# Optimization experiments

Hardware: AMD Instinct MI355X
Metric: run time of the kernel (lower is better)

Reference implementation:

```python
import jax, jax.numpy as jnp
import numpy as np

N_NODES = 16
N_EDGES = 64
N_LAYERS = 4


def _gcn(x, src, dst, emask, W, b):
    # PyG GCNConv: add self-loops, symmetric deg^-1/2 normalization, sum-aggregate.
    n = x.shape[0]
    h = x @ W  # [n, d_out]
    deg = jax.ops.segment_sum(emask, dst, num_segments=n) + 1.0  # +1 self-loop
    dinv = jax.lax.rsqrt(deg)
    norm = dinv[src] * dinv[dst] * emask  # masked-out edges get 0 weight
    out = jax.ops.segment_sum(norm[:, None] * h[src], dst, num_segments=n)
    return out + (dinv * dinv)[:, None] * h + b  # self-loop term + bias


def _sag_pool(x, src, dst, emask, w_rel, b_rel, w_root, k):
    # SAGPooling with GraphConv scorer: score = lin_rel(sum_j x_j) + lin_root(x)
    n = x.shape[0]
    agg = jax.ops.segment_sum(emask[:, None] * x[src], dst, num_segments=n)
    score = agg @ w_rel + b_rel + x @ w_root  # [n]
    perm = jnp.argsort(-score)[:k]  # top-k nodes
    x_new = x[perm] * jnp.tanh(score[perm])[:, None]
    kept = jnp.zeros(n, bool).at[perm].set(True)
    pos = jnp.zeros(n, jnp.int32).at[perm].set(jnp.arange(k, dtype=jnp.int32))
    emask_new = emask * kept[src] * kept[dst]  # drop edges touching removed nodes
    return x_new, pos[src], pos[dst], emask_new


def _conv_gnn(x, src, dst, W0, Ws, bs, pWrel, pbrel, pWroot, linW, linb):
    emask = jnp.ones(src.shape[0], x.dtype)
    n = x.shape[0]
    for i in range(N_LAYERS):
        W = W0 if i == 0 else Ws[i - 1]
        x = jax.nn.relu(_gcn(x, src, dst, emask, W, bs[i]))
        k = -(-n // 2)  # ceil(0.5 * n) -- SAGPooling ratio=0.5
        x, src, dst, emask = _sag_pool(x, src, dst, emask, pWrel[i], pbrel[i], pWroot[i], k)
        n = k
    x = x @ linW + linb  # [1, 128]
    return jax.nn.log_softmax(x, axis=1)


def _fc(h, fcW, fcb, lnw, lnb):
    eps = 1e-5
    for i in range(3):
        h = h @ fcW[i] + fcb[i]
        mu = h.mean(-1, keepdims=True)
        var = ((h - mu) ** 2).mean(-1, keepdims=True)
        h = (h - mu) * jax.lax.rsqrt(var + eps) * lnw[i] + lnb[i]
        h = jax.nn.relu(h)
    return h @ fcW[3] + fcb[3]


def setup_inputs() -> dict:
    key = jax.random.key(0)
    ks = iter(jax.random.split(key, 64))

    def rn(shape, s=0.05):
        return jax.random.normal(next(ks), shape, jnp.float32) * s

    def gnn_params(p):
        return {
            p + '_W0': rn((45, 128)), p + '_W': rn((3, 128, 128)),
            p + '_b': jnp.zeros((4, 128), jnp.float32),
            p + '_pWrel': rn((4, 128)), p + '_pbrel': jnp.zeros((4,), jnp.float32),
            p + '_pWroot': rn((4, 128)),
            p + '_linW': rn((128, 128)), p + '_linb': jnp.zeros((128,), jnp.float32),
        }

    inp = {
        'gp_x': rn((N_NODES, 45), 1.0), 'sp_x': rn((N_NODES, 45), 1.0),
        'gp_src': jax.random.randint(next(ks), (N_EDGES,), 0, N_NODES, jnp.int32),
        'gp_dst': jax.random.randint(next(ks), (N_EDGES,), 0, N_NODES, jnp.int32),
        'sp_src': jax.random.randint(next(ks), (N_EDGES,), 0, N_NODES, jnp.int32),
        'sp_dst': jax.random.randint(next(ks), (N_EDGES,), 0, N_NODES, jnp.int32),
        'fcW': rn((4, 256, 256)), 'fcb': jnp.zeros((4, 256), jnp.float32),
        'lnw': jnp.ones((3, 256), jnp.float32), 'lnb': jnp.zeros((3, 256), jnp.float32),
    }
    inp.update(gnn_params('g'))
    inp.update(gnn_params('s'))
    return inp


def reference(gp_x, sp_x, gp_src, gp_dst, sp_src, sp_dst,
              g_W0, g_W, g_b, g_pWrel, g_pbrel, g_pWroot, g_linW, g_linb,
              s_W0, s_W, s_b, s_pWrel, s_pbrel, s_pWroot, s_linW, s_linb,
              fcW, fcb, lnw, lnb):
    out1 = _conv_gnn(gp_x, gp_src, gp_dst, g_W0, g_W, g_b, g_pWrel, g_pbrel, g_pWroot, g_linW, g_linb)
    out2 = _conv_gnn(sp_x, sp_src, sp_dst, s_W0, s_W, s_b, s_pWrel, s_pbrel, s_pWroot, s_linW, s_linb)
    concat = jnp.concatenate((out1.reshape(-1), out2.reshape(-1)))  # [256]
    return _fc(concat, fcW, fcb, lnw, lnb)
```

## Files before the change

### kernel.cpp

```cpp
#include <hip/hip_runtime.h>
#include <math.h>

#define MAGIC 0x5F3759DFu
typedef unsigned int u32;

__device__ __forceinline__ void bar_lds(){
  asm volatile("s_waitcnt lgkmcnt(0)\n\ts_barrier" ::: "memory");
}
__device__ __forceinline__ void bar_vm0(){
  asm volatile("s_waitcnt vmcnt(0) lgkmcnt(0)\n\ts_barrier" ::: "memory");
}
__device__ __forceinline__ void bar_vm8(){
  asm volatile("s_waitcnt vmcnt(8) lgkmcnt(0)\n\ts_barrier" ::: "memory");
}

__device__ inline float wsum(float v){
  #pragma unroll
  for (int o=32;o;o>>=1) v += __shfl_xor(v,o,64);
  return v;
}
__device__ inline float wmax(float v){
  #pragma unroll
  for (int o=32;o;o>>=1) v = fmaxf(v,__shfl_xor(v,o,64));
  return v;
}
__device__ inline float hsum32(float v){
  #pragma unroll
  for (int o=16;o;o>>=1) v += __shfl_xor(v,o,64);
  return v;
}
__device__ __forceinline__ void stageW(const float* g, float* l, int nfloats,
                                       int wid, int lane){
  const int nch = nfloats>>8;
  for (int c=wid; c<nch; c+=8)
    __builtin_amdgcn_global_load_lds(
      (__attribute__((address_space(1))) u32*)(void*)(g+(c<<8)+(lane<<2)),
      (__attribute__((address_space(3))) u32*)(void*)(l+(c<<8)), 16, 0, 0);
}
__device__ __forceinline__ void pf(const float* p, int nfloats, int tid){
  float4 acc={0.f,0.f,0.f,0.f};
  const int nq=nfloats>>2;
  for (int i=tid;i<nq;i+=512){
    const float4 v=((const float4*)p)[i];
    acc.x+=v.x; acc.y+=v.y; acc.z+=v.z; acc.w+=v.w;
  }
  asm volatile("" :: "v"(acc.x),"v"(acc.y),"v"(acc.z),"v"(acc.w));
}

template<int L>
__device__ __forceinline__ void cfused(int lt, const float* slot, const float* ZBp,
    float (*XB)[128], const float* wrelL, const float* wrootL,
    float4 blv, float* d1P, float* d2P){
  const int SPL=1<<L, CH=128>>L;
  const int o=lt>>L, part=lt&(SPL-1);
  const int v=o>>5, c4=o&31, f0=part*CH;
  const float* zrow = ZBp + v*128;
  float4 a={0.f,0.f,0.f,0.f};
  #pragma unroll
  for (int f=0; f<CH; ++f){
    const float zv=zrow[f0+f];
    const float4 w4=*(const float4*)&slot[(f0+f)*128+(c4<<2)];
    a.x+=zv*w4.x; a.y+=zv*w4.y; a.z+=zv*w4.z; a.w+=zv*w4.w;
  }
  #pragma unroll
  for (int m=1;m<SPL;m<<=1){
    a.x+=__shfl_xor(a.x,m,64); a.y+=__shfl_xor(a.y,m,64);
    a.z+=__shfl_xor(a.z,m,64); a.w+=__shfl_xor(a.w,m,64);
  }
  float p1=0.f,p2=0.f;
  if (part==0){
    float4 ox;
    ox.x=fmaxf(a.x+blv.x,0.f); ox.y=fmaxf(a.y+blv.y,0.f);
    ox.z=fmaxf(a.z+blv.z,0.f); ox.w=fmaxf(a.w+blv.w,0.f);
    *(float4*)&XB[v][c4<<2]=ox;
    const float4 wr4=*(const float4*)&wrelL[(L<<7)+(c4<<2)];
    const float4 wo4=*(const float4*)&wrootL[(L<<7)+(c4<<2)];
    p1=ox.x*wr4.x+ox.y*wr4.y+ox.z*wr4.z+ox.w*wr4.w;
    p2=ox.x*wo4.x+ox.y*wo4.y+ox.z*wo4.z+ox.w*wo4.w;
  }
  p1=wsum(p1); p2=wsum(p2);
  const int wid=lt>>6, lane=lt&63;
  if (lane==0){
    const int vv=wid>>(L-1), wp=wid&((1<<(L-1))-1);
    d1P[(vv<<2)+wp]=p1; d2P[(vv<<2)+wp]=p2;
  }
}

__global__ __launch_bounds__(512,1) void net_kernel(
    const float* __restrict__ gp_x, const float* __restrict__ sp_x,
    const int* __restrict__ gp_src, const int* __restrict__ gp_dst,
    const int* __restrict__ sp_src, const int* __restrict__ sp_dst,
    const float* __restrict__ g_W0, const float* __restrict__ g_W,
    const float* __restrict__ g_b,  const float* __restrict__ g_pWrel,
    const float* __restrict__ g_pbrel, const float* __restrict__ g_pWroot,
    const float* __restrict__ g_linW, const float* __restrict__ g_linb,
    const float* __restrict__ s_W0, const float* __restrict__ s_W,
    const float* __restrict__ s_b,  const float* __restrict__ s_pWrel,
    const float* __restrict__ s_pbrel, const float* __restrict__ s_pWroot,
    const float* __restrict__ s_linW, const float* __restrict__ s_linb,
    const float* __restrict__ fcW, const float* __restrict__ fcb,
    const float* __restrict__ lnw, const float* __restrict__ lnb,
    float* __restrict__ wsbuf, float* __restrict__ out)
{
  __shared__ __align__(16) float slotA[16384];
  __shared__ __align__(16) float slotB[16384];
  __shared__ __align__(16) float XBx[16][128];
  __shared__ __align__(16) float ZBraw[1024];
  __shared__ __align__(16) float wrelL[512], wrootL[512];
  __shared__ __align__(16) float Adn[256], Mdn[256];
  __shared__ float d1P[64], d2P[64];
  __shared__ float yA[128];
  __shared__ float tsA[8]; __shared__ int permA[8];
  __shared__ float fcin[256]; __shared__ float wpart[16];

  const int lt  = threadIdx.x;
  const int bid = blockIdx.x;
  const int wid = lt>>6, lane = lt&63;

  if (bid >= 6){
    switch(bid){
      case 8:  pf(g_W0,5760,lt);        pf(g_W,32768,lt);      break;
      case 9:  pf(s_W0,5760,lt);        pf(s_W,32768,lt);      break;
      case 6:  pf(g_W+32768,16384,lt);  pf(g_linW,16384,lt);
               pf(g_pWrel,512,lt);      pf(g_pWroot,512,lt);   break;
      case 7:  pf(s_W+32768,16384,lt);  pf(s_linW,16384,lt);
               pf(s_pWrel,512,lt);      pf(s_pWroot,512,lt);   break;
      case 10: pf(fcW,65536,lt);        break;
      case 11: pf(fcW+65536,65536,lt);  break;
      case 12: pf(fcW+131072,65536,lt); break;
      case 13: pf(fcW+196608,65536,lt); break;
      case 14: pf(fcb,1024,lt); pf(lnw,768,lt); pf(lnb,768,lt); break;
      default: break;
    }
    return;
  }

  if (bid >= 2){
    const int L = bid-2;
    const int qfc=(wid<<3)+(lane&7), f0fc=(lane>>3)<<5;
    float4 wr[32];
    #pragma unroll
    for (int t=0;t<32;++t) wr[t]=*(const float4*)(fcW+(L<<16)+(f0fc+t)*256+(qfc<<2));
    const float4 bb=*(const float4*)(fcb+(L<<8)+(qfc<<2));
    float4 lw={0,0,0,0}, lb2={0,0,0,0};
    if (L<3){ lw=*(const float4*)(lnw+(L<<8)+(qfc<<2)); lb2=*(const float4*)(lnb+(L<<8)+(qfc<<2)); }
    if (lt==0){
      if (L==0){
        const u32* f1=(const u32*)(wsbuf+128);
        const u32* f2=(const u32*)(wsbuf+384);
        while (__hip_atomic_load(f1,__ATOMIC_ACQUIRE,__HIP_MEMORY_SCOPE_AGENT)!=MAGIC ||
               __hip_atomic_load(f2,__ATOMIC_ACQUIRE,__HIP_MEMORY_SCOPE_AGENT)!=MAGIC)
          __builtin_amdgcn_s_sleep(1);
      } else {
        const u32* f1=(const u32*)(wsbuf+512+(L-1)*512+256);
        while (__hip_atomic_load(f1,__ATOMIC_ACQUIRE,__HIP_MEMORY_SCOPE_AGENT)!=MAGIC)
          __builtin_amdgcn_s_sleep(1);
      }
    }
    bar_lds();
    if (lt<256){
      const float* src = (L==0) ? (wsbuf + (lt<128 ? lt : 128+lt))
                                : (wsbuf + 512 + (L-1)*512 + lt);
      fcin[lt]=__hip_atomic_load(src,__ATOMIC_RELAXED,__HIP_MEMORY_SCOPE_AGENT);
    }
    bar_lds();
    float4 a={0.f,0.f,0.f,0.f};
    #pragma unroll
    for (int t=0;t<32;++t){
      const float zv=fcin[f0fc+t];
      a.x+=zv*wr[t].x; a.y+=zv*wr[t].y; a.z+=zv*wr[t].z; a.w+=zv*wr[t].w;
    }
    #pragma unroll
    for (int m=8;m<64;m<<=1){
      a.x+=__shfl_xor(a.x,m,64); a.y+=__shfl_xor(a.y,m,64);
      a.z+=__shfl_xor(a.z,m,64); a.w+=__shfl_xor(a.w,m,64);
    }
    if (L==3){
      if (lane<8){
        float4 r; r.x=a.x+bb.x; r.y=a.y+bb.y; r.z=a.z+bb.z; r.w=a.w+bb.w;
        *(float4*)(out+(qfc<<2))=r;
      }
      return;
    }
    const bool act=(lane<8);
    float4 hv={0.f,0.f,0.f,0.f};
    if (act){
      hv.x=a.x+bb.x; hv.y=a.y+bb.y; hv.z=a.z+bb.z; hv.w=a.w+bb.w;
      float s=hv.x+hv.y+hv.z+hv.w;
      float s2=hv.x*hv.x+hv.y*hv.y+hv.z*hv.z+hv.w*hv.w;
      #pragma unroll
      for (int m=1;m<8;m<<=1){ s+=__shfl_xor(s,m,64); s2+=__shfl_xor(s2,m,64); }
      if (lane==0){ wpart[wid]=s; wpart[8+wid]=s2; }
    }
    bar_lds();
    if (act){
      float S=0.f,S2=0.f;
      #pragma unroll
      for (int w2=0;w2<8;++w2){ S+=wpart[w2]; S2+=wpart[8+w2]; }
      const float mu=S*(1.f/256.f);
      const float ri=rsqrtf(S2*(1.f/256.f)-mu*mu+1e-5f);
      float* dst=wsbuf+512+L*512+(qfc<<2);
      __hip_atomic_store(dst+0,fmaxf((hv.x-mu)*ri*lw.x+lb2.x,0.f),__ATOMIC_RELAXED,__HIP_MEMORY_SCOPE_AGENT);
      __hip_atomic_store(dst+1,fmaxf((hv.y-mu)*ri*lw.y+lb2.y,0.f),__ATOMIC_RELAXED,__HIP_MEMORY_SCOPE_AGENT);
      __hip_atomic_store(dst+2,fmaxf((hv.z-mu)*ri*lw.z+lb2.z,0.f),__ATOMIC_RELAXED,__HIP_MEMORY_SCOPE_AGENT);
      __hip_atomic_store(dst+3,fmaxf((hv.w-mu)*ri*lw.w+lb2.w,0.f),__ATOMIC_RELAXED,__HIP_MEMORY_SCOPE_AGENT);
    }
    __threadfence();
    bar_lds();
    if (lt==0) __hip_atomic_store((u32*)(wsbuf+512+L*512+256),MAGIC,__ATOMIC_RELEASE,__HIP_MEMORY_SCOPE_AGENT);
    return;
  }

  const int br = bid;
  const float* x0    = br ? sp_x    : gp_x;
  const int*   srcg  = br ? sp_src  : gp_src;
  const int*   dstg  = br ? sp_dst  : gp_dst;
  const float* W0    = br ? s_W0    : g_W0;
  const float* Wl    = br ? s_W     : g_W;
  const float* bl    = br ? s_b     : g_b;
  const float* wrel  = br ? s_pWrel : g_pWrel;
  const float* brel  = br ? s_pbrel : g_pbrel;
  const float* wroot = br ? s_pWroot: g_pWroot;
  const float* linWg = br ? s_linW  : g_linW;
  const float* linb  = br ? s_linb  : g_linb;
  float* wsOut = wsbuf + br*256;
  u32*   wsFlag = (u32*)(wsbuf + 128 + br*256);

  float xv[4];
  #pragma unroll
  for (int r=0;r<4;++r){
    const int i=lt+(r<<9), v=i>>7, f=i&127;
    xv[r] = (f<45)? x0[v*45+f] : 0.f;
  }
  int es=0, ed=0; float emk=0.f;
  if (lt<64){ es=srcg[lt]; ed=dstg[lt]; emk=1.f; }
  const float4 brelv = *(const float4*)brel;
  const float4 blv0=*(const float4*)(bl       + ((lt&31)<<2));
  const float4 blv1=*(const float4*)(bl + 128 + (((lt>>1)&31)<<2));
  const float4 blv2=*(const float4*)(bl + 256 + (((lt>>2)&31)<<2));
  const float4 blv3=*(const float4*)(bl + 384 + (((lt>>3)&31)<<2));
  const float linb_s = linb[lt>>2];
  asm volatile("" ::: "memory");
  stageW(wrel,  wrelL,  512, wid, lane);
  stageW(wroot, wrootL, 512, wid, lane);
  stageW(Wl,    slotA, 16384, wid, lane);

  auto build_dense=[&](int kk, float wlane, bool with_ts){
    const float4 z4={0.f,0.f,0.f,0.f};
    *(float4*)&Adn[lt<<2]=z4;
    *(float4*)&Mdn[lt<<2]=z4;
    const bool act=(emk!=0.f);
    int mycnt=0;
    for (int v=0;v<kk;++v){
      const unsigned long long m=__ballot(act&&(ed==v));
      if (lt==v) mycnt=__popcll(m);
    }
    const float dinvl=rsqrtf(1.f+(float)mycnt);
    const float dvs=__shfl(dinvl,es,64);
    const float dvd=__shfl(dinvl,ed,64);
    if (act){
      atomicAdd(&Adn[ed*16+es], dvs*dvd*wlane);
      atomicAdd(&Mdn[ed*16+es], 1.f);
    }
    if (lt<kk){
      const float tv = with_ts ? tsA[lt] : 1.f;
      atomicAdd(&Adn[lt*17], dinvl*dinvl*tv);
    }
  };
  auto doE=[&](int n,int k,float bv,int nparts,bool rebuild){
    if (lt<64){
      float d1s=0.f, d2s=0.f;
      if (lt<n){
        for (int p=0;p<nparts;++p){ d1s+=d1P[(lt<<2)+p]; d2s+=d2P[(lt<<2)+p]; }
      }
      float sc=-INFINITY;
      if (lt<n){
        float acc=d2s+bv;
        for (int u=0;u<n;++u) acc += Mdn[lt*16+u]*__shfl(d1s,u,64);
        sc=acc;
      }
      int rank=0;
      for (int u=0;u<n;++u){
        const float su=__shfl(sc,u,64);
        rank += (su>sc || (su==sc && u<lt)) ? 1:0;
      }
      const int kept=(lt<n && rank<k)?1:0;
      const int pos=kept?rank:0;
      const float tval=kept?tanhf(sc):0.f;
      if (kept){ permA[rank]=lt; tsA[rank]=tval; }
      const float ts_src=__shfl(tval,es,64);
      const int ks=__shfl(kept,es,64), kd=__shfl(kept,ed,64);
      const int ps=__shfl(pos,es,64),  pd=__shfl(pos,ed,64);
      emk *= (float)(ks&kd);
      es=ps; ed=pd;
      if (rebuild) build_dense(k, ts_src, true);
    }
  };
  auto doB=[&](int n){
    if (lt<(n<<5)){
      const int v=lt>>5, j4=(lt&31)<<2;
      float4 a={0.f,0.f,0.f,0.f};
      for (int u=0;u<n;++u){
        const float w=Adn[v*16+u];
        const float4 xs=*(const float4*)&XBx[permA[u]][j4];
        a.x+=w*xs.x; a.y+=w*xs.y; a.z+=w*xs.z; a.w+=w*xs.w;
      }
      *(float4*)&ZBraw[(v<<7)+j4]=a;
    }
  };

  #pragma unroll
  for (int r=0;r<4;++r){
    const int i=lt+(r<<9), v=i>>7, f=i&127;
    XBx[v][f]=xv[r];
  }
  if (lt<64) build_dense(16, 1.f, false);
  bar_lds();

  if (lt<256){
    const int v=lt>>4, j4=(lt&15)<<2;
    if (j4<48){
      float4 a={0.f,0.f,0.f,0.f};
      for (int u=0;u<16;++u){
        const float w=Adn[v*16+u];
        const float4 xs=*(const float4*)&XBx[u][j4];
        a.x+=w*xs.x; a.y+=w*xs.y; a.z+=w*xs.z; a.w+=w*xs.w;
      }
      *(float4*)&ZBraw[v*48+j4]=a;
    }
  }
  bar_vm8();

  {
    const int v=lt>>5, c4=lt&31, j4=c4<<2;
    const float* zrow=&ZBraw[v*48];
    float4 a={0.f,0.f,0.f,0.f};
    #pragma unroll
    for (int bb=0;bb<2;++bb){
      float4 wr[16]; float zr[16];
      #pragma unroll
      for (int t=0;t<16;++t){ wr[t]=*(const float4*)(W0+(bb*16+t)*128+j4); zr[t]=zrow[bb*16+t]; }
      #pragma unroll
      for (int t=0;t<16;++t){ a.x+=zr[t]*wr[t].x; a.y+=zr[t]*wr[t].y; a.z+=zr[t]*wr[t].z; a.w+=zr[t]*wr[t].w; }
    }
    { float4 wr[13]; float zr[13];
      #pragma unroll
      for (int t=0;t<13;++t){ wr[t]=*(const float4*)(W0+(32+t)*128+j4); zr[t]=zrow[32+t]; }
      #pragma unroll
      for (int t=0;t<13;++t){ a.x+=zr[t]*wr[t].x; a.y+=zr[t]*wr[t].y; a.z+=zr[t]*wr[t].z; a.w+=zr[t]*wr[t].w; }
    }
    float4 ox;
    ox.x=fmaxf(a.x+blv0.x,0.f); ox.y=fmaxf(a.y+blv0.y,0.f);
    ox.z=fmaxf(a.z+blv0.z,0.f); ox.w=fmaxf(a.w+blv0.w,0.f);
    *(float4*)&XBx[v][j4]=ox;
    const float4 wr4=*(const float4*)&wrelL[j4];
    const float4 wo4=*(const float4*)&wrootL[j4];
    float p1=ox.x*wr4.x+ox.y*wr4.y+ox.z*wr4.z+ox.w*wr4.w;
    float p2=ox.x*wo4.x+ox.y*wo4.y+ox.z*wo4.z+ox.w*wo4.w;
    p1=hsum32(p1); p2=hsum32(p2);
    if ((lane&31)==0){
      const int vv=(wid<<1)|(lane>>5);
      d1P[vv<<2]=p1; d2P[vv<<2]=p2;
    }
  }
  stageW(Wl+16384, slotB, 16384, wid, lane);
  bar_lds();

  doE(16, 8, brelv.x, 1, true);  bar_lds();
  doB(8);                        bar_vm8();
  cfused<1>(lt, slotA, ZBraw, XBx, wrelL, wrootL, blv1, d1P, d2P);
  bar_lds();
  stageW(Wl+32768, slotA, 16384, wid, lane);
  doE(8, 4, brelv.y, 1, true);   bar_lds();
  doB(4);                        bar_vm8();
  cfused<2>(lt, slotB, ZBraw, XBx, wrelL, wrootL, blv2, d1P, d2P);
  bar_lds();
  stageW(linWg, slotB, 16384, wid, lane);
  doE(4, 2, brelv.z, 2, true);   bar_lds();
  doB(2);                        bar_vm8();
  cfused<3>(lt, slotA, ZBraw, XBx, wrelL, wrootL, blv3, d1P, d2P);
  bar_lds();
  doE(2, 1, brelv.w, 4, false);  bar_vm0();

  {
    const int oj=lt>>2, fh=lt&3;
    const int prow=permA[0];
    float p=0.f;
    #pragma unroll
    for (int i=0;i<32;++i){
      const int f=(fh<<5)+i;
      p += XBx[prow][f]*slotB[f*128+oj];
    }
    p+=__shfl_xor(p,1,64); p+=__shfl_xor(p,2,64);
    if (fh==0) yA[oj]=p*tsA[0]+linb_s;
  }
  bar_lds();
  if (lt<128){
    const int ln=lt&63;
    const float a0=yA[ln], b0=yA[64+ln];
    const float m=wmax(fmaxf(a0,b0));
    const float sum=wsum(expf(a0-m)+expf(b0-m));
    const float lse=m+logf(sum);
    __hip_atomic_store(&wsOut[lt], yA[lt]-lse, __ATOMIC_RELAXED, __HIP_MEMORY_SCOPE_AGENT);
  }
  __threadfence();
  bar_lds();
  if (lt==0) __hip_atomic_store(wsFlag, MAGIC, __ATOMIC_RELEASE, __HIP_MEMORY_SCOPE_AGENT);
}

extern "C" void kernel_launch(void* const* d_in, const int* in_sizes, int n_in,
                              void* d_out, int out_size, void* d_ws, size_t ws_size,
                              hipStream_t stream){
  net_kernel<<<16,512,0,stream>>>(
    (const float*)d_in[0],(const float*)d_in[1],
    (const int*)d_in[2],(const int*)d_in[3],(const int*)d_in[4],(const int*)d_in[5],
    (const float*)d_in[10],(const float*)d_in[11],(const float*)d_in[12],(const float*)d_in[13],
    (const float*)d_in[14],(const float*)d_in[15],(const float*)d_in[16],(const float*)d_in[17],
    (const float*)d_in[18],(const float*)d_in[19],(const float*)d_in[20],(const float*)d_in[21],
    (const float*)d_in[22],(const float*)d_in[23],(const float*)d_in[24],(const float*)d_in[25],
    (const float*)d_in[6],(const float*)d_in[7],(const float*)d_in[8],(const float*)d_in[9],
    (float*)d_ws,(float*)d_out);
}
```

Baseline: 27.41 us.

## Split per-layer GCN matvec into LDS partial-sum pass and reduce pass; reshard prefetch blocks

The fused per-layer transform, which reduced split-K partials with cross-lane shuffles and a wave-sum, is replaced by two phases. Each thread first writes its partial float4 into a new LDS buffer, then a second pass sums the partials, applies bias and ReLU, and computes the pooling score dot products. This removes the multi-part score accumulation in the top-k step but adds one barrier and an LDS round trip per layer. The prefetch (cache-warming) blocks are redistributed across 20 blocks so they touch the GNN weights and biases in smaller chunks, and they no longer touch the FC weights.

```diff
diff --git a/kernel.cpp b/kernel.cpp
--- a/kernel.cpp
+++ b/kernel.cpp
@@ -45,45 +45,6 @@
     acc.x+=v.x; acc.y+=v.y; acc.z+=v.z; acc.w+=v.w;
   }
   asm volatile("" :: "v"(acc.x),"v"(acc.y),"v"(acc.z),"v"(acc.w));
-}
-
-template<int L>
-__device__ __forceinline__ void cfused(int lt, const float* slot, const float* ZBp,
-    float (*XB)[128], const float* wrelL, const float* wrootL,
-    float4 blv, float* d1P, float* d2P){
-  const int SPL=1<<L, CH=128>>L;
-  const int o=lt>>L, part=lt&(SPL-1);
-  const int v=o>>5, c4=o&31, f0=part*CH;
-  const float* zrow = ZBp + v*128;
-  float4 a={0.f,0.f,0.f,0.f};
-  #pragma unroll
-  for (int f=0; f<CH; ++f){
-    const float zv=zrow[f0+f];
-    const float4 w4=*(const float4*)&slot[(f0+f)*128+(c4<<2)];
-    a.x+=zv*w4.x; a.y+=zv*w4.y; a.z+=zv*w4.z; a.w+=zv*w4.w;
-  }
-  #pragma unroll
-  for (int m=1;m<SPL;m<<=1){
-    a.x+=__shfl_xor(a.x,m,64); a.y+=__shfl_xor(a.y,m,64);
-    a.z+=__shfl_xor(a.z,m,64); a.w+=__shfl_xor(a.w,m,64);
-  }
-  float p1=0.f,p2=0.f;
-  if (part==0){
-    float4 ox;
-    ox.x=fmaxf(a.x+blv.x,0.f); ox.y=fmaxf(a.y+blv.y,0.f);
-    ox.z=fmaxf(a.z+blv.z,0.f); ox.w=fmaxf(a.w+blv.w,0.f);
-    *(float4*)&XB[v][c4<<2]=ox;
-    const float4 wr4=*(const float4*)&wrelL[(L<<7)+(c4<<2)];
-    const float4 wo4=*(const float4*)&wrootL[(L<<7)+(c4<<2)];
-    p1=ox.x*wr4.x+ox.y*wr4.y+ox.z*wr4.z+ox.w*wr4.w;
-    p2=ox.x*wo4.x+ox.y*wo4.y+ox.z*wo4.z+ox.w*wo4.w;
-  }
-  p1=wsum(p1); p2=wsum(p2);
-  const int wid=lt>>6, lane=lt&63;
-  if (lane==0){
-    const int vv=wid>>(L-1), wp=wid&((1<<(L-1))-1);
-    d1P[(vv<<2)+wp]=p1; d2P[(vv<<2)+wp]=p2;
-  }
 }
 
 __global__ __launch_bounds__(512,1) void net_kernel(
@@ -106,6 +67,7 @@
   __shared__ __align__(16) float slotB[16384];
   __shared__ __align__(16) float XBx[16][128];
   __shared__ __align__(16) float ZBraw[1024];
+  __shared__ __align__(16) float PBf[2048];
   __shared__ __align__(16) float wrelL[512], wrootL[512];
   __shared__ __align__(16) float Adn[256], Mdn[256];
   __shared__ float d1P[64], d2P[64];
@@ -118,20 +80,14 @@
   const int wid = lt>>6, lane = lt&63;
 
   if (bid >= 6){
-    switch(bid){
-      case 8:  pf(g_W0,5760,lt);        pf(g_W,32768,lt);      break;
-      case 9:  pf(s_W0,5760,lt);        pf(s_W,32768,lt);      break;
-      case 6:  pf(g_W+32768,16384,lt);  pf(g_linW,16384,lt);
-               pf(g_pWrel,512,lt);      pf(g_pWroot,512,lt);   break;
-      case 7:  pf(s_W+32768,16384,lt);  pf(s_linW,16384,lt);
-               pf(s_pWrel,512,lt);      pf(s_pWroot,512,lt);   break;
-      case 10: pf(fcW,65536,lt);        break;
-      case 11: pf(fcW+65536,65536,lt);  break;
-      case 12: pf(fcW+131072,65536,lt); break;
-      case 13: pf(fcW+196608,65536,lt); break;
-      case 14: pf(fcb,1024,lt); pf(lnw,768,lt); pf(lnb,768,lt); break;
-      default: break;
-    }
+    if (bid==6){ pf(g_W0,5760,lt); pf(g_pWrel,512,lt); pf(g_pWroot,512,lt);
+                 pf(g_b,512,lt);   pf(g_linb,128,lt); }
+    else if (bid==7){ pf(s_W0,5760,lt); pf(s_pWrel,512,lt); pf(s_pWroot,512,lt);
+                 pf(s_b,512,lt);   pf(s_linb,128,lt); }
+    else if (bid<=11) pf(g_W + (bid-8)*12288, 12288, lt);
+    else if (bid<=15) pf(s_W + (bid-12)*12288, 12288, lt);
+    else if (bid<=17) pf(g_linW + (bid-16)*8192, 8192, lt);
+    else              pf(s_linW + (bid-18)*8192, 8192, lt);
     return;
   }
 
@@ -235,10 +191,11 @@
   int es=0, ed=0; float emk=0.f;
   if (lt<64){ es=srcg[lt]; ed=dstg[lt]; emk=1.f; }
   const float4 brelv = *(const float4*)brel;
-  const float4 blv0=*(const float4*)(bl       + ((lt&31)<<2));
-  const float4 blv1=*(const float4*)(bl + 128 + (((lt>>1)&31)<<2));
-  const float4 blv2=*(const float4*)(bl + 256 + (((lt>>2)&31)<<2));
-  const float4 blv3=*(const float4*)(bl + 384 + (((lt>>3)&31)<<2));
+  const int bi4=(lt&31)<<2;
+  const float4 blv0=*(const float4*)(bl       + bi4);
+  const float4 blv1=*(const float4*)(bl + 128 + bi4);
+  const float4 blv2=*(const float4*)(bl + 256 + bi4);
+  const float4 blv3=*(const float4*)(bl + 384 + bi4);
   const float linb_s = linb[lt>>2];
   asm volatile("" ::: "memory");
   stageW(wrel,  wrelL,  512, wid, lane);
@@ -267,15 +224,12 @@
       atomicAdd(&Adn[lt*17], dinvl*dinvl*tv);
     }
   };
-  auto doE=[&](int n,int k,float bv,int nparts,bool rebuild){
+  auto doE=[&](int n,int k,float bv,bool rebuild){
     if (lt<64){
-      float d1s=0.f, d2s=0.f;
-      if (lt<n){
-        for (int p=0;p<nparts;++p){ d1s+=d1P[(lt<<2)+p]; d2s+=d2P[(lt<<2)+p]; }
-      }
+      const float d1s=(lt<n)? d1P[lt<<2] : 0.f;
       float sc=-INFINITY;
       if (lt<n){
-        float acc=d2s+bv;
+        float acc=d2P[lt<<2]+bv;
         for (int u=0;u<n;++u) acc += Mdn[lt*16+u]*__shfl(d1s,u,64);
         sc=acc;
       }
@@ -306,6 +260,40 @@
         a.x+=w*xs.x; a.y+=w*xs.y; a.z+=w*xs.z; a.w+=w*xs.w;
       }
       *(float4*)&ZBraw[(v<<7)+j4]=a;
+    }
+  };
+  auto cmain=[&](const float* slot, int L){
+    const int sh=9-L, nq=512>>L, CH=128>>L;
+    const int q=lt&(nq-1), fh=lt>>sh;
+    const int v=q>>5, c4=q&31, f0=fh*CH;
+    const float* zrow=&ZBraw[v<<7];
+    float4 a={0.f,0.f,0.f,0.f};
+    for (int f=0; f<CH; ++f){
+      const float zv=zrow[f0+f];
+      const float4 w4=*(const float4*)&slot[(f0+f)*128+(c4<<2)];
+      a.x+=zv*w4.x; a.y+=zv*w4.y; a.z+=zv*w4.z; a.w+=zv*w4.w;
+    }
+    ((float4*)PBf)[lt]=a;
+  };
+  auto creduce=[&](int L, float4 bl4){
+    const int nq=512>>L, SPL=1<<L;
+    if (lt<nq){
+      const int v=lt>>5, c4=lt&31;
+      float4 acc=bl4;
+      for (int s=0;s<SPL;++s){
+        const float4 p=((const float4*)PBf)[s*nq+lt];
+        acc.x+=p.x; acc.y+=p.y; acc.z+=p.z; acc.w+=p.w;
+      }
+      float4 o;
+      o.x=fmaxf(acc.x,0.f); o.y=fmaxf(acc.y,0.f);
+      o.z=fmaxf(acc.z,0.f); o.w=fmaxf(acc.w,0.f);
+      *(float4*)&XBx[v][c4<<2]=o;
+      const float4 wr4=*(const float4*)&wrelL[(L<<7)+(c4<<2)];
+      const float4 wo4=*(const float4*)&wrootL[(L<<7)+(c4<<2)];
+      float p1=o.x*wr4.x+o.y*wr4.y+o.z*wr4.z+o.w*wr4.w;
+      float p2=o.x*wo4.x+o.y*wo4.y+o.z*wo4.z+o.w*wo4.w;
+      p1=hsum32(p1); p2=hsum32(p2);
+      if ((lane&31)==0){ d1P[v<<2]=p1; d2P[v<<2]=p2; }
     }
   };
 
@@ -366,21 +354,21 @@
   stageW(Wl+16384, slotB, 16384, wid, lane);
   bar_lds();
 
-  doE(16, 8, brelv.x, 1, true);  bar_lds();
-  doB(8);                        bar_vm8();
-  cfused<1>(lt, slotA, ZBraw, XBx, wrelL, wrootL, blv1, d1P, d2P);
-  bar_lds();
+  doE(16, 8, brelv.x, true);   bar_lds();
+  doB(8);                      bar_vm8();
+  cmain(slotA, 1);             bar_lds();
+  creduce(1, blv1);            bar_lds();
   stageW(Wl+32768, slotA, 16384, wid, lane);
-  doE(8, 4, brelv.y, 1, true);   bar_lds();
-  doB(4);                        bar_vm8();
-  cfused<2>(lt, slotB, ZBraw, XBx, wrelL, wrootL, blv2, d1P, d2P);
-  bar_lds();
+  doE(8, 4, brelv.y, true);    bar_lds();
+  doB(4);                      bar_vm8();
+  cmain(slotB, 2);             bar_lds();
+  creduce(2, blv2);            bar_lds();
   stageW(linWg, slotB, 16384, wid, lane);
-  doE(4, 2, brelv.z, 2, true);   bar_lds();
-  doB(2);                        bar_vm8();
-  cfused<3>(lt, slotA, ZBraw, XBx, wrelL, wrootL, blv3, d1P, d2P);
-  bar_lds();
-  doE(2, 1, brelv.w, 4, false);  bar_vm0();
+  doE(4, 2, brelv.z, true);    bar_lds();
+  doB(2);                      bar_vm8();
+  cmain(slotA, 3);             bar_lds();
+  creduce(3, blv3);            bar_lds();
+  doE(2, 1, brelv.w, false);   bar_vm0();
 
   {
     const int oj=lt>>2, fh=lt&3;
@@ -411,7 +399,7 @@
 extern "C" void kernel_launch(void* const* d_in, const int* in_sizes, int n_in,
                               void* d_out, int out_size, void* d_ws, size_t ws_size,
                               hipStream_t stream){
-  net_kernel<<<16,512,0,stream>>>(
+  net_kernel<<<20,512,0,stream>>>(
     (const float*)d_in[0],(const float*)d_in[1],
     (const int*)d_in[2],(const int*)d_in[3],(const int*)d_in[4],(const int*)d_in[5],
     (const float*)d_in[10],(const float*)d_in[11],(const float*)d_in[12],(const float*)d_in[13],
```

Measured after the change: 24.18 us. -11.8%, faster.
